# Kernel optimization log

Hardware: AMD Instinct MI355X
Metric: run time of the kernel (lower is better)

Reference implementation:

```python
import jax, jax.numpy as jnp
import numpy as np

B, S, D, H, E = 2, 2048, 1024, 4096, 8


def setup_inputs() -> dict:
    key = jax.random.key(0)
    k0, k1, k2, k3 = jax.random.split(key, 4)
    x = jax.random.normal(k0, (B, S, D), dtype=jnp.float32)
    router_w = jax.random.normal(k1, (E, D), dtype=jnp.float32) * 0.02   # Top2Router Linear weight [E, D]
    w1 = jax.random.normal(k2, (E, D, H), dtype=jnp.float32) * 0.02      # stacked fc1 weights (transposed: x @ w1[e])
    w2 = jax.random.normal(k3, (E, H, D), dtype=jnp.float32) * 0.02      # stacked fc2 weights
    return {"x": x, "router_w": router_w, "w1": w1, "w2": w2}


def reference(x, router_w, w1, w2):
    # x: [B, S, D] -> flatten tokens. Single-rank EP: all-to-all is identity,
    # microbatch split is a pure overlap trick, per-token math unchanged.
    b, s, d = x.shape
    e = router_w.shape[0]
    xf = x.reshape(-1, d)                                     # [T, D]
    # Top-2 router with renormalized gate weights
    probs = jax.nn.softmax(xf @ router_w.T, axis=-1)          # [T, E]
    topv, topi = jax.lax.top_k(probs, 2)                      # [T, 2]
    topv = topv / (topv.sum(axis=-1, keepdims=True) + 1e-9)
    # Combine weights per expert: cw[t,e] = sum_k topv[t,k] * [topi[t,k]==e]
    cw = (jax.nn.one_hot(topi, e, dtype=xf.dtype) * topv[..., None]).sum(axis=1)  # [T, E]
    # Expert MLPs (dense-over-experts reference for the grouped GEMM)
    h = jax.nn.gelu(jnp.einsum('td,edh->teh', xf, w1), approximate=False)  # [T, E, H]
    y = jnp.einsum('teh,ehd->ted', h, w2)                                   # [T, E, D]
    out = jnp.einsum('te,ted->td', cw, y)                                   # weighted combine (scatter-add equiv.)
    return out.reshape(b, s, d)
```

## Files before the change

kernel.cpp:

```cpp
#include <hip/hip_runtime.h>

#define T_TOK 4096
#define DIM   1024
#define HID   4096
#define NEXP  8
#define MAXROWS 9216

typedef unsigned short u16;
typedef __attribute__((ext_vector_type(8))) short short8;
typedef __attribute__((ext_vector_type(4))) float f32x4;
typedef __attribute__((ext_vector_type(2))) unsigned short u16x2;
typedef __attribute__((ext_vector_type(4))) unsigned short u16x4;
typedef __attribute__((ext_vector_type(8))) unsigned short u16x8;

typedef __attribute__((address_space(3))) unsigned int lds_uint;
typedef const __attribute__((address_space(1))) unsigned int gbl_uint;

__device__ __forceinline__ u16 f2bf(float f) {
    union { float f; unsigned int u; } v; v.f = f;
    unsigned int r = v.u + 0x7fffu + ((v.u >> 16) & 1u);
    return (u16)(r >> 16);
}

__device__ __forceinline__ float gelu_f(float v) {
    float u = 1.5957691216f * (v + 0.044715f * v * v * v);
    float s = 1.0f / (1.0f + __expf(-u));
    return v * s;
}

__global__ __launch_bounds__(256)
void transpose_cast2(const float* __restrict__ w1, u16* __restrict__ w1t,
                     const float* __restrict__ w2, u16* __restrict__ w2t,
                     int* __restrict__ counts) {
    int b = blockIdx.x;
    if (b == 0 && threadIdx.x < NEXP) counts[threadIdx.x] = 0;
    const float* in; u16* out; int R, C, bx, by, e;
    if (b < 2048) {
        e = b >> 8; int t = b & 255; bx = t & 31; by = t >> 5;
        in = w1; out = w1t; R = DIM; C = HID;
    } else {
        b -= 2048;
        e = b >> 8; int t = b & 255; bx = t & 7; by = t >> 3;
        in = w2; out = w2t; R = HID; C = DIM;
    }
    __shared__ u16 tl[128 * 130];
    size_t mo = (size_t)e * DIM * HID;
    const float* ip = in + mo;
    u16* op = out + mo;
    int c0 = bx * 128, r0 = by * 128;
    int tid = threadIdx.x;
#pragma unroll
    for (int j = 0; j < 16; ++j) {
        int id = tid + 256 * j;
        int r = id >> 5, cg = id & 31;
        f32x4 v = *(const f32x4*)(ip + (size_t)(r0 + r) * C + c0 + 4 * cg);
        u16x2 wa; wa.x = f2bf(v.x); wa.y = f2bf(v.y);
        u16x2 wb; wb.x = f2bf(v.z); wb.y = f2bf(v.w);
        *(u16x2*)(tl + r * 130 + 4 * cg)     = wa;
        *(u16x2*)(tl + r * 130 + 4 * cg + 2) = wb;
    }
    __syncthreads();
#pragma unroll
    for (int j = 0; j < 8; ++j) {
        int id = tid + 256 * j;
        int c = id >> 4, ch = id & 15;
        u16x8 o;
#pragma unroll
        for (int k = 0; k < 8; ++k) o[k] = tl[(ch * 8 + k) * 130 + c];
        *(u16x8*)(op + (size_t)(c0 + c) * R + r0 + ch * 8) = o;
    }
}

__global__ __launch_bounds__(256)
void router_k(const float* __restrict__ x, const float* __restrict__ rw,
              int* __restrict__ counts, int* __restrict__ tE,
              int* __restrict__ tS, float* __restrict__ tG) {
    int wave = threadIdx.x >> 6, lane = threadIdx.x & 63;
    int t = blockIdx.x * 4 + wave;
    const float* xr = x + (size_t)t * DIM;
    float xv[16];
#pragma unroll
    for (int i = 0; i < 16; ++i) xv[i] = xr[lane + 64*i];
    float lg[NEXP];
#pragma unroll
    for (int e = 0; e < NEXP; ++e) {
        const float* wr_ = rw + e * DIM;
        float a = 0.f;
#pragma unroll
        for (int i = 0; i < 16; ++i) a += xv[i] * wr_[lane + 64*i];
        lg[e] = a;
    }
#pragma unroll
    for (int off = 32; off > 0; off >>= 1)
#pragma unroll
        for (int e = 0; e < NEXP; ++e) lg[e] += __shfl_xor(lg[e], off, 64);
    if (lane == 0) {
        float mx = lg[0];
        for (int e = 1; e < NEXP; ++e) mx = fmaxf(mx, lg[e]);
        float p[NEXP], s = 0.f;
        for (int e = 0; e < NEXP; ++e) { p[e] = expf(lg[e] - mx); s += p[e]; }
        float inv_s = 1.f / s;
        for (int e = 0; e < NEXP; ++e) p[e] *= inv_s;
        int i0 = 0;
        for (int e = 1; e < NEXP; ++e) if (p[e] > p[i0]) i0 = e;
        int i1 = (i0 == 0) ? 1 : 0;
        for (int e = 0; e < NEXP; ++e) if (e != i0 && p[e] > p[i1]) i1 = e;
        float v0 = p[i0], v1 = p[i1];
        float inv = 1.f / (v0 + v1 + 1e-9f);
        int s0 = atomicAdd(&counts[i0], 1);
        int s1 = atomicAdd(&counts[i1], 1);
        tE[2*t] = i0;  tE[2*t+1] = i1;
        tS[2*t] = s0;  tS[2*t+1] = s1;
        tG[2*t] = v0 * inv;  tG[2*t+1] = v1 * inv;
    }
}

__device__ __forceinline__ int pbase_of(const int* __restrict__ counts, int e) {
    int pb = 0;
#pragma unroll
    for (int i = 0; i < NEXP; ++i) {
        int pad = ((counts[i] + 127) >> 7) << 7;
        pb += (i < e) ? pad : 0;
    }
    return pb;
}

__global__ __launch_bounds__(256)
void gather_k(const float* __restrict__ x, const int* __restrict__ tE,
              const int* __restrict__ tS, const int* __restrict__ counts,
              u16* __restrict__ xg) {
    int a = blockIdx.x;
    int t = a >> 1, k = a & 1;
    int e = tE[2*t + k];
    int row = pbase_of(counts, e) + tS[2*t + k];
    const f32x4* xr = (const f32x4*)(x + (size_t)t * DIM);
    u16x4* o = (u16x4*)(xg + (size_t)row * DIM);
    int i = threadIdx.x;
    f32x4 v = xr[i];
    u16x4 r; r.x = f2bf(v.x); r.y = f2bf(v.y); r.z = f2bf(v.z); r.w = f2bf(v.w);
    o[i] = r;
}

template<int K, int KSPLIT, bool GELU, typename OutT>
__global__ __launch_bounds__(512, 2)
void gemm_bt(const u16* __restrict__ A, const u16* __restrict__ BtAll,
             OutT* __restrict__ C, const int* __restrict__ counts,
             int N, size_t cstride) {
    int e  = blockIdx.z / KSPLIT;
    int ks = blockIdx.z % KSPLIT;
    int cnt = counts[e];
    int mt = blockIdx.y;
    if (mt * 256 >= cnt) return;
    int row0 = pbase_of(counts, e) + mt * 256;
    int limit = cnt - mt * 256;
    const u16* Bt = BtAll + (size_t)e * N * K;
    OutT* Cp = C + (size_t)ks * cstride;
    int col0 = blockIdx.x * 256;
    const int kb0 = ks * (K / KSPLIT);
    constexpr int NT = K / KSPLIT / 64;

    __shared__ __align__(16) u16 smem[65536];

    int tid = threadIdx.x;
    int lane = tid & 63;
    int w = tid >> 6;
    int quad = lane >> 4, m16 = lane & 15;
    int wr = (w >> 2) * 128, wc = (w & 3) * 64;
    int rsub = lane >> 3;
    int kch  = lane & 7;
    int kchs = kch ^ rsub;

    const u16* ga[4];
    const u16* gb[4];
#pragma unroll
    for (int i = 0; i < 4; ++i) {
        int g = (w << 2) + i;
        int ra = row0 + g * 8 + rsub;
        if (ra > MAXROWS - 1) ra = MAXROWS - 1;
        ga[i] = A  + (size_t)ra * K + kb0 + kchs * 8;
        gb[i] = Bt + (size_t)(col0 + g * 8 + rsub) * K + kb0 + kchs * 8;
    }
    int sw = m16 & 7;
    const int aoff = (wr + m16) * 64;
    const int boff = (wc + m16) * 64;
    const int c0lo = (quad ^ sw) << 3;
    const int c0hi = ((4 + quad) ^ sw) << 3;

    f32x4 acc[8][4] = {};

#pragma unroll
    for (int i = 0; i < 4; ++i) {
        int g = (w << 2) + i;
        __builtin_amdgcn_global_load_lds((gbl_uint*)ga[i], (lds_uint*)(smem + g * 512), 16, 0, 0);
        __builtin_amdgcn_global_load_lds((gbl_uint*)gb[i], (lds_uint*)(smem + 32768 + g * 512), 16, 0, 0);
        ga[i] += 64; gb[i] += 64;
    }
    asm volatile("s_waitcnt vmcnt(0)" ::: "memory");
    __builtin_amdgcn_s_barrier();

#pragma unroll 2
    for (int t = 0; t < NT; ++t) {
        const u16* Ab = smem + (t & 1) * 16384;
        const u16* Bb = smem + 32768 + (t & 1) * 16384;
        short8 a0[4], a1[4], b0[4], b1[4];
        if (t + 1 < NT) {
#pragma unroll
            for (int i = 0; i < 4; ++i) {
                int g = (w << 2) + i;
                __builtin_amdgcn_global_load_lds((gbl_uint*)ga[i],
                    (lds_uint*)(smem + ((t + 1) & 1) * 16384 + g * 512), 16, 0, 0);
                __builtin_amdgcn_global_load_lds((gbl_uint*)gb[i],
                    (lds_uint*)(smem + 32768 + ((t + 1) & 1) * 16384 + g * 512), 16, 0, 0);
                ga[i] += 64; gb[i] += 64;
            }
        }
#pragma unroll
        for (int m = 0; m < 4; ++m) {
            a0[m] = *(const short8*)(Ab + aoff + m * 1024 + c0lo);
            a1[m] = *(const short8*)(Ab + aoff + m * 1024 + c0hi);
        }
#pragma unroll
        for (int n = 0; n < 2; ++n) {
            b0[n] = *(const short8*)(Bb + boff + n * 1024 + c0lo);
            b1[n] = *(const short8*)(Bb + boff + n * 1024 + c0hi);
        }
        __builtin_amdgcn_s_barrier();
        asm volatile("s_waitcnt lgkmcnt(0)" ::: "memory");
        __builtin_amdgcn_s_setprio(1);
#pragma unroll
        for (int m = 0; m < 4; ++m)
#pragma unroll
            for (int n = 0; n < 2; ++n) {
                acc[m][n] = __builtin_amdgcn_mfma_f32_16x16x32_bf16(a0[m], b0[n], acc[m][n], 0, 0, 0);
                acc[m][n] = __builtin_amdgcn_mfma_f32_16x16x32_bf16(a1[m], b1[n], acc[m][n], 0, 0, 0);
            }
        __builtin_amdgcn_s_setprio(0);
        __builtin_amdgcn_s_barrier();
#pragma unroll
        for (int n = 2; n < 4; ++n) {
            b0[n] = *(const short8*)(Bb + boff + n * 1024 + c0lo);
            b1[n] = *(const short8*)(Bb + boff + n * 1024 + c0hi);
        }
        __builtin_amdgcn_s_barrier();
        asm volatile("s_waitcnt lgkmcnt(0)" ::: "memory");
        __builtin_amdgcn_s_setprio(1);
#pragma unroll
        for (int m = 0; m < 4; ++m)
#pragma unroll
            for (int n = 2; n < 4; ++n) {
                acc[m][n] = __builtin_amdgcn_mfma_f32_16x16x32_bf16(a0[m], b0[n], acc[m][n], 0, 0, 0);
                acc[m][n] = __builtin_amdgcn_mfma_f32_16x16x32_bf16(a1[m], b1[n], acc[m][n], 0, 0, 0);
            }
        __builtin_amdgcn_s_setprio(0);
        __builtin_amdgcn_s_barrier();
#pragma unroll
        for (int m = 0; m < 4; ++m) {
            a0[m] = *(const short8*)(Ab + aoff + (4 + m) * 1024 + c0lo);
            a1[m] = *(const short8*)(Ab + aoff + (4 + m) * 1024 + c0hi);
        }
        __builtin_amdgcn_s_barrier();
        asm volatile("s_waitcnt lgkmcnt(0)" ::: "memory");
        __builtin_amdgcn_s_setprio(1);
#pragma unroll
        for (int m = 0; m < 4; ++m)
#pragma unroll
            for (int n = 2; n < 4; ++n) {
                acc[4 + m][n] = __builtin_amdgcn_mfma_f32_16x16x32_bf16(a0[m], b0[n], acc[4 + m][n], 0, 0, 0);
                acc[4 + m][n] = __builtin_amdgcn_mfma_f32_16x16x32_bf16(a1[m], b1[n], acc[4 + m][n], 0, 0, 0);
            }
        __builtin_amdgcn_s_setprio(0);
        __builtin_amdgcn_s_barrier();
        __builtin_amdgcn_s_setprio(1);
#pragma unroll
        for (int m = 0; m < 4; ++m)
#pragma unroll
            for (int n = 0; n < 2; ++n) {
                acc[4 + m][n] = __builtin_amdgcn_mfma_f32_16x16x32_bf16(a0[m], b0[n], acc[4 + m][n], 0, 0, 0);
                acc[4 + m][n] = __builtin_amdgcn_mfma_f32_16x16x32_bf16(a1[m], b1[n], acc[4 + m][n], 0, 0, 0);
            }
        __builtin_amdgcn_s_setprio(0);
        asm volatile("s_waitcnt vmcnt(0)" ::: "memory");
        __builtin_amdgcn_s_barrier();
    }

    if (GELU) {
#pragma unroll
        for (int mi = 0; mi < 8; ++mi) {
#pragma unroll
            for (int r = 0; r < 4; ++r) {
                int row = wr + mi * 16 + quad * 4 + r;
#pragma unroll
                for (int ni = 0; ni < 4; ++ni) {
                    int col = wc + ni * 16 + m16;
                    int ch = col >> 3, w8 = col & 7;
                    smem[row * 256 + (((ch ^ (row & 31)) << 3) | w8)] = f2bf(gelu_f(acc[mi][ni][r]));
                }
            }
        }
        __syncthreads();
        int rr = tid >> 5, ch = tid & 31;
#pragma unroll
        for (int it = 0; it < 16; ++it) {
            int row = it * 16 + rr;
            if (row < limit) {
                u16x8 v = *(const u16x8*)(smem + row * 256 + ((ch ^ (row & 31)) << 3));
                *(u16x8*)((u16*)Cp + (size_t)(row0 + row) * N + col0 + ch * 8) = v;
            }
        }
    } else {
#pragma unroll
        for (int mi = 0; mi < 8; ++mi)
#pragma unroll
            for (int r = 0; r < 4; ++r) {
                int rl = wr + mi * 16 + quad * 4 + r;
                if (rl < limit) {
                    float* rp = (float*)Cp + (size_t)(row0 + rl) * N + col0 + wc + m16;
#pragma unroll
                    for (int ni = 0; ni < 4; ++ni)
                        rp[ni * 16] = acc[mi][ni][r];
                }
            }
    }
}

__global__ __launch_bounds__(256)
void combine_k(const float* __restrict__ p0, const float* __restrict__ p1,
               const int* __restrict__ tE, const int* __restrict__ tS,
               const float* __restrict__ tG, const int* __restrict__ counts,
               float* __restrict__ out) {
    int t = blockIdx.x;
    int e0 = tE[2*t], e1 = tE[2*t+1];
    int r0 = pbase_of(counts, e0) + tS[2*t];
    int r1 = pbase_of(counts, e1) + tS[2*t+1];
    float g0 = tG[2*t], g1 = tG[2*t+1];
    int i = threadIdx.x;
    f32x4 a0 = ((const f32x4*)(p0 + (size_t)r0 * DIM))[i];
    f32x4 b0 = ((const f32x4*)(p1 + (size_t)r0 * DIM))[i];
    f32x4 a1 = ((const f32x4*)(p0 + (size_t)r1 * DIM))[i];
    f32x4 b1 = ((const f32x4*)(p1 + (size_t)r1 * DIM))[i];
    f32x4* o = (f32x4*)(out + (size_t)t * DIM);
    o[i] = g0 * (a0 + b0) + g1 * (a1 + b1);
}

extern "C" void kernel_launch(void* const* d_in, const int* in_sizes, int n_in,
                              void* d_out, int out_size, void* d_ws, size_t ws_size,
                              hipStream_t stream) {
    const float* x  = (const float*)d_in[0];
    const float* rw = (const float*)d_in[1];
    const float* w1 = (const float*)d_in[2];
    const float* w2 = (const float*)d_in[3];
    float* out = (float*)d_out;

    char* ws = (char*)d_ws;
    u16* w1t = (u16*)(ws + 0);
    u16* xg  = (u16*)(ws + 67108864ull);
    u16* w2t = (u16*)(ws + 85983232ull);
    u16* hb  = (u16*)(ws + 153092096ull);
    float* p0 = (float*)(ws + 0);
    float* p1 = (float*)(ws + 37748736ull);
    int* ctrl   = (int*)(ws + 228589568ull);
    int* counts = ctrl;
    int* tE     = ctrl + 32;
    int* tS     = ctrl + 32 + 8192;
    float* tG   = (float*)(ctrl + 32 + 16384);

    transpose_cast2<<<4096, 256, 0, stream>>>(w1, w1t, w2, w2t, counts);
    router_k<<<T_TOK / 4, 256, 0, stream>>>(x, rw, counts, tE, tS, tG);
    gather_k<<<T_TOK * 2, 256, 0, stream>>>(x, tE, tS, counts, xg);
    gemm_bt<DIM, 1, true, u16><<<dim3(HID / 256, 16, NEXP), 512, 0, stream>>>(
        xg, w1t, hb, counts, HID, 0);
    gemm_bt<HID, 2, false, float><<<dim3(DIM / 256, 16, NEXP * 2), 512, 0, stream>>>(
        hb, w2t, p0, counts, DIM, (size_t)MAXROWS * DIM);
    combine_k<<<T_TOK, 256, 0, stream>>>(p0, p1, tE, tS, tG, counts, out);
}
```

Baseline: 698.7 us.

## Swizzle GEMM workgroup order across XCDs and cut per-iteration barriers

Result: slower. 730.6 us (+4.6%).

```diff
diff --git a/kernel.cpp b/kernel.cpp
--- a/kernel.cpp
+++ b/kernel.cpp
@@ -141,21 +141,28 @@
     o[i] = r;
 }
 
-template<int K, int KSPLIT, bool GELU, typename OutT>
+template<int K, int KSPLIT, int NX, bool GELU, typename OutT>
 __global__ __launch_bounds__(512, 2)
 void gemm_bt(const u16* __restrict__ A, const u16* __restrict__ BtAll,
              OutT* __restrict__ C, const int* __restrict__ counts,
              int N, size_t cstride) {
-    int e  = blockIdx.z / KSPLIT;
-    int ks = blockIdx.z % KSPLIT;
+    int bid = blockIdx.x;
+    constexpr int NWG = NX * 16 * NEXP * KSPLIT;
+    int swz = (bid & 7) * (NWG / 8) + (bid >> 3);
+    int mt = swz & 15;
+    int tmp = swz >> 4;
+    int xb, z;
+    if constexpr (NX == 16) { xb = tmp & 15; z = tmp >> 4; }
+    else                    { xb = tmp & 3;  z = tmp >> 2; }
+    int e  = z / KSPLIT;
+    int ks = z % KSPLIT;
     int cnt = counts[e];
-    int mt = blockIdx.y;
     if (mt * 256 >= cnt) return;
     int row0 = pbase_of(counts, e) + mt * 256;
     int limit = cnt - mt * 256;
     const u16* Bt = BtAll + (size_t)e * N * K;
     OutT* Cp = C + (size_t)ks * cstride;
-    int col0 = blockIdx.x * 256;
+    int col0 = xb * 256;
     const int kb0 = ks * (K / KSPLIT);
     constexpr int NT = K / KSPLIT / 64;
 
@@ -195,14 +202,12 @@
         __builtin_amdgcn_global_load_lds((gbl_uint*)gb[i], (lds_uint*)(smem + 32768 + g * 512), 16, 0, 0);
         ga[i] += 64; gb[i] += 64;
     }
-    asm volatile("s_waitcnt vmcnt(0)" ::: "memory");
-    __builtin_amdgcn_s_barrier();
 
 #pragma unroll 2
     for (int t = 0; t < NT; ++t) {
         const u16* Ab = smem + (t & 1) * 16384;
         const u16* Bb = smem + 32768 + (t & 1) * 16384;
-        short8 a0[4], a1[4], b0[4], b1[4];
+        __builtin_amdgcn_s_barrier();
         if (t + 1 < NT) {
 #pragma unroll
             for (int i = 0; i < 4; ++i) {
@@ -213,7 +218,14 @@
                     (lds_uint*)(smem + 32768 + ((t + 1) & 1) * 16384 + g * 512), 16, 0, 0);
                 ga[i] += 64; gb[i] += 64;
             }
-        }
+            asm volatile("s_waitcnt vmcnt(8)" ::: "memory");
+        } else {
+            asm volatile("s_waitcnt vmcnt(0)" ::: "memory");
+        }
+        __builtin_amdgcn_s_barrier();
+        __builtin_amdgcn_sched_barrier(0);
+
+        short8 a0[4], a1[4], b0[4], b1[4];
 #pragma unroll
         for (int m = 0; m < 4; ++m) {
             a0[m] = *(const short8*)(Ab + aoff + m * 1024 + c0lo);
@@ -224,8 +236,6 @@
             b0[n] = *(const short8*)(Bb + boff + n * 1024 + c0lo);
             b1[n] = *(const short8*)(Bb + boff + n * 1024 + c0hi);
         }
-        __builtin_amdgcn_s_barrier();
-        asm volatile("s_waitcnt lgkmcnt(0)" ::: "memory");
         __builtin_amdgcn_s_setprio(1);
 #pragma unroll
         for (int m = 0; m < 4; ++m)
@@ -235,14 +245,11 @@
                 acc[m][n] = __builtin_amdgcn_mfma_f32_16x16x32_bf16(a1[m], b1[n], acc[m][n], 0, 0, 0);
             }
         __builtin_amdgcn_s_setprio(0);
-        __builtin_amdgcn_s_barrier();
 #pragma unroll
         for (int n = 2; n < 4; ++n) {
             b0[n] = *(const short8*)(Bb + boff + n * 1024 + c0lo);
             b1[n] = *(const short8*)(Bb + boff + n * 1024 + c0hi);
         }
-        __builtin_amdgcn_s_barrier();
-        asm volatile("s_waitcnt lgkmcnt(0)" ::: "memory");
         __builtin_amdgcn_s_setprio(1);
 #pragma unroll
         for (int m = 0; m < 4; ++m)
@@ -252,14 +259,11 @@
                 acc[m][n] = __builtin_amdgcn_mfma_f32_16x16x32_bf16(a1[m], b1[n], acc[m][n], 0, 0, 0);
             }
         __builtin_amdgcn_s_setprio(0);
-        __builtin_amdgcn_s_barrier();
 #pragma unroll
         for (int m = 0; m < 4; ++m) {
             a0[m] = *(const short8*)(Ab + aoff + (4 + m) * 1024 + c0lo);
             a1[m] = *(const short8*)(Ab + aoff + (4 + m) * 1024 + c0hi);
         }
-        __builtin_amdgcn_s_barrier();
-        asm volatile("s_waitcnt lgkmcnt(0)" ::: "memory");
         __builtin_amdgcn_s_setprio(1);
 #pragma unroll
         for (int m = 0; m < 4; ++m)
@@ -269,7 +273,6 @@
                 acc[4 + m][n] = __builtin_amdgcn_mfma_f32_16x16x32_bf16(a1[m], b1[n], acc[4 + m][n], 0, 0, 0);
             }
         __builtin_amdgcn_s_setprio(0);
-        __builtin_amdgcn_s_barrier();
         __builtin_amdgcn_s_setprio(1);
 #pragma unroll
         for (int m = 0; m < 4; ++m)
@@ -279,11 +282,10 @@
                 acc[4 + m][n] = __builtin_amdgcn_mfma_f32_16x16x32_bf16(a1[m], b1[n], acc[4 + m][n], 0, 0, 0);
             }
         __builtin_amdgcn_s_setprio(0);
-        asm volatile("s_waitcnt vmcnt(0)" ::: "memory");
-        __builtin_amdgcn_s_barrier();
     }
 
     if (GELU) {
+        __syncthreads();
 #pragma unroll
         for (int mi = 0; mi < 8; ++mi) {
 #pragma unroll
@@ -367,9 +369,9 @@
     transpose_cast2<<<4096, 256, 0, stream>>>(w1, w1t, w2, w2t, counts);
     router_k<<<T_TOK / 4, 256, 0, stream>>>(x, rw, counts, tE, tS, tG);
     gather_k<<<T_TOK * 2, 256, 0, stream>>>(x, tE, tS, counts, xg);
-    gemm_bt<DIM, 1, true, u16><<<dim3(HID / 256, 16, NEXP), 512, 0, stream>>>(
+    gemm_bt<DIM, 1, 16, true, u16><<<2048, 512, 0, stream>>>(
         xg, w1t, hb, counts, HID, 0);
-    gemm_bt<HID, 2, false, float><<<dim3(DIM / 256, 16, NEXP * 2), 512, 0, stream>>>(
+    gemm_bt<HID, 2, 4, false, float><<<1024, 512, 0, stream>>>(
         hb, w2t, p0, counts, DIM, (size_t)MAXROWS * DIM);
     combine_k<<<T_TOK, 256, 0, stream>>>(p0, p1, tE, tS, tG, counts, out);
 }
```
